# Kernel tuning notes

Hardware: AMD Instinct MI355X
Metric: run time of the kernel (lower is better)

Reference implementation:

```python
import jax, jax.numpy as jnp
import numpy as np

N = 50000        # nodes
E = 800000       # original edges (no self loops)
HEADS = 2
OUT = 64         # hidden_channels
NUM_GRAPHS = 128
NEG_SLOPE = 0.2


def setup_inputs() -> dict:
    key = jax.random.key(0)
    ks = jax.random.split(key, 16)
    # edge_index guaranteed free of self loops (remove_self_loops then add_self_loops
    # in the original makes the final edge set = original edges + N self loops)
    src = jax.random.randint(ks[0], (E,), 0, N)
    off = jax.random.randint(ks[1], (E,), 1, N)
    dst = (src + off) % N
    edge_index = jnp.stack([src, dst]).astype(jnp.int64)
    batch = jnp.sort(jax.random.randint(ks[2], (N,), 0, NUM_GRAPHS)).astype(jnp.int64)
    def glorot(k, shape):
        fan = shape[-1] + (shape[0] if len(shape) > 1 else shape[-1])
        s = jnp.sqrt(6.0 / fan)
        return jax.random.uniform(k, shape, jnp.float32, -s, s)
    return {
        "x": jax.random.normal(ks[3], (N, 128), jnp.float32),
        "edge_index": edge_index,
        "batch": batch,
        "node_centrality": jax.random.uniform(ks[4], (N,), jnp.float32),
        "edge_centrality": jax.random.uniform(ks[5], (E,), jnp.float32),
        "W0": glorot(ks[6], (128, HEADS * OUT)),
        "as0": glorot(ks[7], (HEADS, OUT)),
        "ad0": glorot(ks[8], (HEADS, OUT)),
        "b0": jnp.ones((HEADS * OUT,), jnp.float32),
        "W1": glorot(ks[9], (HEADS * OUT, HEADS * OUT)),
        "as1": glorot(ks[10], (HEADS, OUT)),
        "ad1": glorot(ks[11], (HEADS, OUT)),
        "b1": jnp.ones((HEADS * OUT,), jnp.float32),
        "Wc": glorot(ks[12], (HEADS * OUT, 10)),
        "bc": jnp.zeros((10,), jnp.float32),
    }


def qgat_layer(x, src, dst, norm_quantum, W, a_src, a_dst, b):
    # x: [N, Cin]; src/dst: [E+N]; norm_quantum: [E+N]
    h = (x @ W).reshape(N, HEADS, OUT)                      # [N,H,D]
    alpha_s = jnp.einsum('nhd,hd->nh', h, a_src)            # [N,H]
    alpha_d = jnp.einsum('nhd,hd->nh', h, a_dst)
    alpha = jax.nn.leaky_relu(alpha_s[src] + alpha_d[dst], NEG_SLOPE)  # [E+N,H]
    # segment softmax over destination node (every node has a self loop)
    amax = jax.ops.segment_max(alpha, dst, num_segments=N)
    amax = jnp.where(jnp.isfinite(amax), amax, 0.0)
    ex = jnp.exp(alpha - amax[dst])
    denom = jax.ops.segment_sum(ex, dst, num_segments=N)
    attn = ex / (denom[dst] + 1e-16)                        # [E+N,H]
    # message: norm_quantum * alpha * x_j, scatter-add to dst
    msg = norm_quantum[:, None, None] * attn[:, :, None] * h[src]
    out = jax.ops.segment_sum(msg, dst, num_segments=N)     # [N,H,D]
    return jax.nn.relu(out.reshape(N, HEADS * OUT) + b)


def reference(x, edge_index, batch, node_centrality, edge_centrality,
              W0, as0, ad0, b0, W1, as1, ad1, b1, Wc, bc):
    loop = jnp.arange(N, dtype=edge_index.dtype)
    src = jnp.concatenate([edge_index[0], loop])            # self loops appended
    dst = jnp.concatenate([edge_index[1], loop])
    nq = jnp.concatenate([edge_centrality, node_centrality])  # [E+N]
    # eval mode: dropout is identity
    h = qgat_layer(x, src, dst, nq, W0, as0, ad0, b0)
    h = qgat_layer(h, src, dst, nq, W1, as1, ad1, b1)
    # global mean pool over graphs in the batch
    sums = jax.ops.segment_sum(h, batch, num_segments=NUM_GRAPHS)
    cnts = jax.ops.segment_sum(jnp.ones((N,), h.dtype), batch, num_segments=NUM_GRAPHS)
    pooled = sums / jnp.maximum(cnts, 1.0)[:, None]         # [G, H*D]
    return pooled @ Wc + bc                                  # [G, 10]
```

## Files before the change

### kernel.cpp

```cpp
#include <hip/hip_runtime.h>

#define N_NODES 50000
#define E_EDGES 800000
#define EA (E_EDGES + N_NODES)
#define NG 128
#define NEG 0.2f
#define NB_SCAN ((N_NODES + 255) / 256)
#define PCH 64

typedef _Float16 half8  __attribute__((ext_vector_type(8)));
typedef _Float16 half2t __attribute__((ext_vector_type(2)));
typedef float    floatx4 __attribute__((ext_vector_type(4)));

__device__ __forceinline__ half2t h2bits(unsigned u) { return __builtin_bit_cast(half2t, u); }

__global__ void init_kernel(const float* __restrict__ W0, const float* __restrict__ W1,
                            _Float16* __restrict__ Wt0, _Float16* __restrict__ Wt1,
                            int* __restrict__ deg, float* __restrict__ sums) {
    int i = blockIdx.x * 256 + threadIdx.x;
    if (i < N_NODES) deg[i] = 0;
    if (i < NG * 128) sums[i] = 0.f;
    if (i < 16384) {
        int c = i >> 7, k = i & 127;
        Wt0[c * 128 + k] = (_Float16)W0[k * 128 + c];
        Wt1[c * 128 + k] = (_Float16)W1[k * 128 + c];
    }
}

__global__ void hist_kernel(const int* __restrict__ ei, int* __restrict__ deg,
                            int* __restrict__ rank) {
    int e = blockIdx.x * blockDim.x + threadIdx.x;
    if (e >= EA) return;
    int d = (e < E_EDGES) ? ei[E_EDGES + e] : (e - E_EDGES);
    rank[e] = atomicAdd(&deg[d], 1);
}

__global__ void partial_kernel(const int* __restrict__ deg, int* __restrict__ part) {
    __shared__ int buf[4];
    int i = blockIdx.x * 256 + threadIdx.x;
    int v = (i < N_NODES) ? deg[i] : 0;
    for (int o = 32; o; o >>= 1) v += __shfl_xor(v, o);
    if ((threadIdx.x & 63) == 0) buf[threadIdx.x >> 6] = v;
    __syncthreads();
    if (threadIdx.x == 0) part[blockIdx.x] = buf[0] + buf[1] + buf[2] + buf[3];
}

__global__ void rowstart_kernel(const int* __restrict__ deg, const int* __restrict__ part,
                                int* __restrict__ rowstart) {
    __shared__ int buf[256];
    __shared__ int wsum[4];
    __shared__ int offs;
    int t = threadIdx.x;
    int pv = (t < blockIdx.x) ? part[t] : 0;
    for (int o = 32; o; o >>= 1) pv += __shfl_xor(pv, o);
    if ((t & 63) == 0) wsum[t >> 6] = pv;
    __syncthreads();
    if (t == 0) offs = wsum[0] + wsum[1] + wsum[2] + wsum[3];
    int i = blockIdx.x * 256 + t;
    int v = (i < N_NODES) ? deg[i] : 0;
    buf[t] = v;
    __syncthreads();
    for (int o = 1; o < 256; o <<= 1) {
        int u = (t >= o) ? buf[t - o] : 0;
        __syncthreads();
        buf[t] += u;
        __syncthreads();
    }
    if (i < N_NODES) rowstart[i] = offs + buf[t] - v;
    if (i == N_NODES - 1) rowstart[N_NODES] = offs + buf[t];
}

__global__ void build_kernel(const int* __restrict__ ei, const float* __restrict__ ec,
                             const float* __restrict__ nc, const int* __restrict__ rowstart,
                             const int* __restrict__ rank, uint2* __restrict__ csr2) {
    int e = blockIdx.x * blockDim.x + threadIdx.x;
    if (e >= EA) return;
    int s, d; float nq;
    if (e < E_EDGES) { s = ei[e]; d = ei[E_EDGES + e]; nq = ec[e]; }
    else             { s = e - E_EDGES; d = s; nq = nc[s]; }
    csr2[rowstart[d] + rank[e]] = make_uint2((unsigned)s, __float_as_uint(nq));
}

template<int SRC_F32>
__global__ __launch_bounds__(256) void gemm_mfma(const void* __restrict__ Xsrc,
                                                 const _Float16* __restrict__ Wt,
                                                 const float* __restrict__ as_,
                                                 const float* __restrict__ ad_,
                                                 unsigned* __restrict__ Hb,
                                                 float* __restrict__ als,
                                                 float* __restrict__ ald) {
    __shared__ _Float16 As[64][136];
    __shared__ _Float16 Bs[128 * 128];
    __shared__ float als_s[4][64];
    __shared__ float ald_s[4][64];
    const int tid = threadIdx.x;
    const int row0 = blockIdx.x * 64;

    if (SRC_F32) {
        const float* X = (const float*)Xsrc;
        for (int i = 0; i < 8; ++i) {
            int idx = tid + i * 256;
            int r = idx >> 5, q = idx & 31;
            int gr = row0 + r;
            float4 v = make_float4(0.f, 0.f, 0.f, 0.f);
            if (gr < N_NODES) v = ((const float4*)X)[(size_t)gr * 32 + q];
            half2t p0 = { (_Float16)v.x, (_Float16)v.y };
            half2t p1 = { (_Float16)v.z, (_Float16)v.w };
            *(half2t*)&As[r][q * 4]     = p0;
            *(half2t*)&As[r][q * 4 + 2] = p1;
        }
    } else {
        const uint4* X = (const uint4*)Xsrc;
        for (int i = 0; i < 4; ++i) {
            int idx = tid + i * 256;
            int r = idx >> 4, q = idx & 15;
            int gr = row0 + r;
            uint4 v = make_uint4(0u, 0u, 0u, 0u);
            if (gr < N_NODES) v = X[(size_t)gr * 16 + q];
            *(uint4*)&As[r][q * 8] = v;
        }
    }
    for (int i = 0; i < 8; ++i) {
        int idx = tid + i * 256;
        int r = idx >> 4, q = idx & 15;
        *(uint4*)&Bs[r * 128 + ((q ^ (r & 15)) << 3)] = ((const uint4*)Wt)[r * 16 + q];
    }
    __syncthreads();

    const int l = tid & 63, wv = tid >> 6;
    const int c0w = wv * 32;
    const int lr = l & 15, lq = l >> 4;

    floatx4 acc[4][2];
#pragma unroll
    for (int m = 0; m < 4; ++m)
#pragma unroll
        for (int n = 0; n < 2; ++n) acc[m][n] = (floatx4){0.f, 0.f, 0.f, 0.f};

#pragma unroll
    for (int kk = 0; kk < 4; ++kk) {
        int kb = kk * 32 + lq * 8;
        int kg = (kk * 4 + lq) ^ lr;
        half8 a0 = *(const half8*)&As[lr][kb];
        half8 a1 = *(const half8*)&As[16 + lr][kb];
        half8 a2 = *(const half8*)&As[32 + lr][kb];
        half8 a3 = *(const half8*)&As[48 + lr][kb];
        half8 b0 = *(const half8*)&Bs[(c0w + lr) * 128 + (kg << 3)];
        half8 b1 = *(const half8*)&Bs[(c0w + 16 + lr) * 128 + (kg << 3)];
        acc[0][0] = __builtin_amdgcn_mfma_f32_16x16x32_f16(a0, b0, acc[0][0], 0, 0, 0);
        acc[1][0] = __builtin_amdgcn_mfma_f32_16x16x32_f16(a1, b0, acc[1][0], 0, 0, 0);
        acc[2][0] = __builtin_amdgcn_mfma_f32_16x16x32_f16(a2, b0, acc[2][0], 0, 0, 0);
        acc[3][0] = __builtin_amdgcn_mfma_f32_16x16x32_f16(a3, b0, acc[3][0], 0, 0, 0);
        acc[0][1] = __builtin_amdgcn_mfma_f32_16x16x32_f16(a0, b1, acc[0][1], 0, 0, 0);
        acc[1][1] = __builtin_amdgcn_mfma_f32_16x16x32_f16(a1, b1, acc[1][1], 0, 0, 0);
        acc[2][1] = __builtin_amdgcn_mfma_f32_16x16x32_f16(a2, b1, acc[2][1], 0, 0, 0);
        acc[3][1] = __builtin_amdgcn_mfma_f32_16x16x32_f16(a3, b1, acc[3][1], 0, 0, 0);
    }

    __syncthreads();

    float asv0 = as_[c0w + lr],      adv0 = ad_[c0w + lr];
    float asv1 = as_[c0w + 16 + lr], adv1 = ad_[c0w + 16 + lr];
#pragma unroll
    for (int m = 0; m < 4; ++m) {
#pragma unroll
        for (int reg = 0; reg < 4; ++reg) {
            float v0 = acc[m][0][reg];
            float v1 = acc[m][1][reg];
            int rl = 16 * m + 4 * lq + reg;
            _Float16* rowp = &As[rl][0];
            rowp[c0w + lr]      = (_Float16)v0;
            rowp[c0w + 16 + lr] = (_Float16)v1;
            float ss = v0 * asv0 + v1 * asv1;
            float dd = v0 * adv0 + v1 * adv1;
            ss += __shfl_xor(ss, 1); dd += __shfl_xor(dd, 1);
            ss += __shfl_xor(ss, 2); dd += __shfl_xor(dd, 2);
            ss += __shfl_xor(ss, 4); dd += __shfl_xor(dd, 4);
            ss += __shfl_xor(ss, 8); dd += __shfl_xor(dd, 8);
            if (lr == 0) { als_s[wv][rl] = ss; ald_s[wv][rl] = dd; }
        }
    }
    __syncthreads();

    for (int i = 0; i < 4; ++i) {
        int idx = tid + i * 256;
        int r = idx >> 4, q = idx & 15;
        int grow = row0 + r;
        if (grow < N_NODES) {
            uint4 v = *(uint4*)((unsigned short*)&As[r][0] + q * 8);
            ((uint4*)Hb)[(size_t)grow * 16 + q] = v;
        }
    }
    int r = tid & 63, sel = tid >> 6;
    int grow = row0 + r;
    if (grow < N_NODES) {
        if (sel == 0)      als[grow * 2 + 0] = als_s[0][r] + als_s[1][r];
        else if (sel == 1) als[grow * 2 + 1] = als_s[2][r] + als_s[3][r];
        else if (sel == 2) ald[grow * 2 + 0] = ald_s[0][r] + ald_s[1][r];
        else               ald[grow * 2 + 1] = ald_s[2][r] + ald_s[3][r];
    }
}

__global__ __launch_bounds__(256) void agg_kernel(const uint4* __restrict__ Hb4,
                                                  const uint2* __restrict__ csr2,
                                                  const float* __restrict__ als,
                                                  const float* __restrict__ ald,
                                                  const int* __restrict__ rowstart,
                                                  const float* __restrict__ bias,
                                                  _Float16* __restrict__ outp) {
    __shared__ uint4 sw[4][64];
    const int wv = threadIdx.x >> 6;
    int n = blockIdx.x * 4 + wv;
    if (n >= N_NODES) return;
    const int lane = threadIdx.x & 63;
    int start = rowstart[n], end = rowstart[n + 1];
    int deg = end - start;
    const float2* als2 = (const float2*)als;
    float2 adn = ((const float2*)ald)[n];

    int   s_reg  = n;
    float nq_reg = 0.f, a0_reg = -1e30f, a1_reg = -1e30f;
    if (lane < deg) {
        uint2 v = csr2[start + lane];
        s_reg  = (int)v.x;
        nq_reg = __uint_as_float(v.y);
        float2 av = als2[s_reg];
        float a0 = av.x + adn.x; a0_reg = (a0 > 0.f) ? a0 : NEG * a0;
        float a1 = av.y + adn.y; a1_reg = (a1 > 0.f) ? a1 : NEG * a1;
    }
    float m0 = a0_reg, m1 = a1_reg;
    for (int i = start + 64 + lane; i < end; i += 64) {
        uint2 v = csr2[i];
        float2 av = als2[v.x];
        float a0 = av.x + adn.x; a0 = (a0 > 0.f) ? a0 : NEG * a0;
        float a1 = av.y + adn.y; a1 = (a1 > 0.f) ? a1 : NEG * a1;
        m0 = fmaxf(m0, a0); m1 = fmaxf(m1, a1);
    }
    for (int o = 32; o; o >>= 1) { m0 = fmaxf(m0, __shfl_xor(m0, o)); m1 = fmaxf(m1, __shfl_xor(m1, o)); }

    float e0 = __expf(a0_reg - m0), e1 = __expf(a1_reg - m1);
    float s0 = e0, s1 = e1;
    for (int i = start + 64 + lane; i < end; i += 64) {
        uint2 v = csr2[i];
        float2 av = als2[v.x];
        float a0 = av.x + adn.x; a0 = (a0 > 0.f) ? a0 : NEG * a0;
        float a1 = av.y + adn.y; a1 = (a1 > 0.f) ? a1 : NEG * a1;
        s0 += __expf(a0 - m0); s1 += __expf(a1 - m1);
    }
    for (int o = 32; o; o >>= 1) { s0 += __shfl_xor(s0, o); s1 += __shfl_xor(s1, o); }
    float inv0 = 1.f / (s0 + 1e-16f), inv1 = 1.f / (s1 + 1e-16f);

    sw[wv][lane] = make_uint4((unsigned)s_reg,
                              __float_as_uint(nq_reg * e0 * inv0),
                              __float_as_uint(nq_reg * e1 * inv1), 0u);

    const int  c16   = lane & 15;
    const int  g     = lane >> 4;
    const bool head0 = (c16 < 8);
    float acc0 = 0.f, acc1 = 0.f, acc2 = 0.f, acc3 = 0.f;
    float acc4 = 0.f, acc5 = 0.f, acc6 = 0.f, acc7 = 0.f;
    int cnt4 = (deg < 64) ? ((deg + 3) & ~3) : 64;
#pragma unroll 4
    for (int jp = 0; jp < cnt4; jp += 4) {
        uint4 sv = sw[wv][jp + g];
        float w  = __uint_as_float(head0 ? sv.y : sv.z);
        uint4 hv = Hb4[(size_t)(sv.x * 16u + (unsigned)c16)];
        half2t h0 = h2bits(hv.x), h1 = h2bits(hv.y), h2 = h2bits(hv.z), h3 = h2bits(hv.w);
        acc0 += (float)h0.x * w; acc1 += (float)h0.y * w;
        acc2 += (float)h1.x * w; acc3 += (float)h1.y * w;
        acc4 += (float)h2.x * w; acc5 += (float)h2.y * w;
        acc6 += (float)h3.x * w; acc7 += (float)h3.y * w;
    }
    for (int cbase = start + 64; cbase < end; cbase += 64) {
        int   s2 = n; float w0f = 0.f, w1f = 0.f;
        int i = cbase + lane;
        if (i < end) {
            uint2 v = csr2[i];
            s2 = (int)v.x;
            float nq = __uint_as_float(v.y);
            float2 av = als2[s2];
            float a0 = av.x + adn.x; a0 = (a0 > 0.f) ? a0 : NEG * a0;
            float a1 = av.y + adn.y; a1 = (a1 > 0.f) ? a1 : NEG * a1;
            w0f = nq * __expf(a0 - m0) * inv0;
            w1f = nq * __expf(a1 - m1) * inv1;
        }
        sw[wv][lane] = make_uint4((unsigned)s2, __float_as_uint(w0f), __float_as_uint(w1f), 0u);
        int rem = end - cbase; if (rem > 64) rem = 64;
        int r4 = (rem + 3) & ~3;
        for (int jp = 0; jp < r4; jp += 4) {
            uint4 sv = sw[wv][jp + g];
            float w  = __uint_as_float(head0 ? sv.y : sv.z);
            uint4 hv = Hb4[(size_t)(sv.x * 16u + (unsigned)c16)];
            half2t h0 = h2bits(hv.x), h1 = h2bits(hv.y), h2 = h2bits(hv.z), h3 = h2bits(hv.w);
            acc0 += (float)h0.x * w; acc1 += (float)h0.y * w;
            acc2 += (float)h1.x * w; acc3 += (float)h1.y * w;
            acc4 += (float)h2.x * w; acc5 += (float)h2.y * w;
            acc6 += (float)h3.x * w; acc7 += (float)h3.y * w;
        }
    }
    acc0 += __shfl_xor(acc0, 16); acc1 += __shfl_xor(acc1, 16);
    acc2 += __shfl_xor(acc2, 16); acc3 += __shfl_xor(acc3, 16);
    acc4 += __shfl_xor(acc4, 16); acc5 += __shfl_xor(acc5, 16);
    acc6 += __shfl_xor(acc6, 16); acc7 += __shfl_xor(acc7, 16);
    acc0 += __shfl_xor(acc0, 32); acc1 += __shfl_xor(acc1, 32);
    acc2 += __shfl_xor(acc2, 32); acc3 += __shfl_xor(acc3, 32);
    acc4 += __shfl_xor(acc4, 32); acc5 += __shfl_xor(acc5, 32);
    acc6 += __shfl_xor(acc6, 32); acc7 += __shfl_xor(acc7, 32);

    if (g == 0) {
        float4 ba = ((const float4*)bias)[c16 * 2];
        float4 bb = ((const float4*)bias)[c16 * 2 + 1];
        float o0 = acc0 + ba.x; o0 = o0 > 0.f ? o0 : 0.f;
        float o1 = acc1 + ba.y; o1 = o1 > 0.f ? o1 : 0.f;
        float o2 = acc2 + ba.z; o2 = o2 > 0.f ? o2 : 0.f;
        float o3 = acc3 + ba.w; o3 = o3 > 0.f ? o3 : 0.f;
        float o4 = acc4 + bb.x; o4 = o4 > 0.f ? o4 : 0.f;
        float o5 = acc5 + bb.y; o5 = o5 > 0.f ? o5 : 0.f;
        float o6 = acc6 + bb.z; o6 = o6 > 0.f ? o6 : 0.f;
        float o7 = acc7 + bb.w; o7 = o7 > 0.f ? o7 : 0.f;
        half8 hv = { (_Float16)o0, (_Float16)o1, (_Float16)o2, (_Float16)o3,
                     (_Float16)o4, (_Float16)o5, (_Float16)o6, (_Float16)o7 };
        *(half8*)(outp + (size_t)n * 128 + 8 * c16) = hv;
    }
}

__global__ __launch_bounds__(256) void pool_partial(const half2t* __restrict__ Obh,
                                                    const int* __restrict__ batch,
                                                    float* __restrict__ sums) {
    int row0 = blockIdx.x * PCH;
    int c2 = threadIdx.x & 63;
    int r4 = threadIdx.x >> 6;
    int end = row0 + PCH; if (end > N_NODES) end = N_NODES;
    float a0 = 0.f, a1 = 0.f;
    int curg = -1;
    for (int i = row0 + r4; i < end; i += 4) {
        int g = batch[i];
        if (g != curg) {
            if (curg >= 0) {
                atomicAdd(&sums[curg * 128 + 2 * c2],     a0);
                atomicAdd(&sums[curg * 128 + 2 * c2 + 1], a1);
            }
            a0 = 0.f; a1 = 0.f; curg = g;
        }
        half2t hv = Obh[(size_t)i * 64 + c2];
        a0 += (float)hv.x;
        a1 += (float)hv.y;
    }
    if (curg >= 0) {
        atomicAdd(&sums[curg * 128 + 2 * c2],     a0);
        atomicAdd(&sums[curg * 128 + 2 * c2 + 1], a1);
    }
}

__global__ void cls_kernel(const float* __restrict__ sums, const int* __restrict__ batch,
                           const float* __restrict__ Wc, const float* __restrict__ bc,
                           float* __restrict__ outp) {
    int g = blockIdx.x;
    __shared__ float p[128];
    __shared__ int cnt_s;
    if (threadIdx.x == 0) {
        int lo = 0, hi = N_NODES;
        while (lo < hi) { int mid = (lo + hi) >> 1; if (batch[mid] < g) lo = mid + 1; else hi = mid; }
        int start = lo;
        hi = N_NODES;
        while (lo < hi) { int mid = (lo + hi) >> 1; if (batch[mid] <= g) lo = mid + 1; else hi = mid; }
        cnt_s = lo - start;
    }
    __syncthreads();
    float inv = 1.f / fmaxf((float)cnt_s, 1.f);
    p[threadIdx.x] = sums[g * 128 + threadIdx.x] * inv;
    __syncthreads();
    if (threadIdx.x < 10) {
        float acc = bc[threadIdx.x];
        for (int k = 0; k < 128; ++k) acc += p[k] * Wc[k * 10 + threadIdx.x];
        outp[g * 10 + threadIdx.x] = acc;
    }
}

extern "C" void kernel_launch(void* const* d_in, const int* in_sizes, int n_in,
                              void* d_out, int out_size, void* d_ws, size_t ws_size,
                              hipStream_t stream) {
    const float* x     = (const float*)d_in[0];
    const int*   ei    = (const int*)d_in[1];
    const int*   batch = (const int*)d_in[2];
    const float* nc    = (const float*)d_in[3];
    const float* ec    = (const float*)d_in[4];
    const float* W0    = (const float*)d_in[5];
    const float* as0   = (const float*)d_in[6];
    const float* ad0   = (const float*)d_in[7];
    const float* b0    = (const float*)d_in[8];
    const float* W1    = (const float*)d_in[9];
    const float* as1   = (const float*)d_in[10];
    const float* ad1   = (const float*)d_in[11];
    const float* b1    = (const float*)d_in[12];
    const float* Wc    = (const float*)d_in[13];
    const float* bc    = (const float*)d_in[14];
    float* out = (float*)d_out;

    char* ws = (char*)d_ws;
    size_t off = 0;
    auto alloc = [&](size_t bytes) { void* p = ws + off; off += (bytes + 255) & ~size_t(255); return p; };
    unsigned*  Hb       = (unsigned*)alloc(sizeof(unsigned) * N_NODES * 64);
    _Float16*  Xh       = (_Float16*)alloc(sizeof(_Float16) * N_NODES * 128);
    _Float16*  Ob       = (_Float16*)alloc(sizeof(_Float16) * N_NODES * 128);
    float*     als      = (float*)alloc(sizeof(float) * N_NODES * 2);
    float*     ald      = (float*)alloc(sizeof(float) * N_NODES * 2);
    _Float16*  Wt0      = (_Float16*)alloc(sizeof(_Float16) * 128 * 128);
    _Float16*  Wt1      = (_Float16*)alloc(sizeof(_Float16) * 128 * 128);
    int*       deg      = (int*)alloc(sizeof(int) * N_NODES);
    int*       rank     = (int*)alloc(sizeof(int) * EA);
    int*       part     = (int*)alloc(sizeof(int) * NB_SCAN);
    int*       rowstart = (int*)alloc(sizeof(int) * (N_NODES + 1));
    uint2*     csr2     = (uint2*)alloc(sizeof(uint2) * EA);
    float*     sums     = (float*)alloc(sizeof(float) * NG * 128);

    init_kernel<<<NB_SCAN, 256, 0, stream>>>(W0, W1, Wt0, Wt1, deg, sums);
    hist_kernel<<<(EA + 255) / 256, 256, 0, stream>>>(ei, deg, rank);
    partial_kernel<<<NB_SCAN, 256, 0, stream>>>(deg, part);
    rowstart_kernel<<<NB_SCAN, 256, 0, stream>>>(deg, part, rowstart);
    build_kernel<<<(EA + 255) / 256, 256, 0, stream>>>(ei, ec, nc, rowstart, rank, csr2);

    int gemm_grid   = (N_NODES + 63) / 64;
    int nwaveblocks = (N_NODES + 3) / 4;

    gemm_mfma<1><<<gemm_grid, 256, 0, stream>>>(x, Wt0, as0, ad0, Hb, als, ald);
    agg_kernel<<<nwaveblocks, 256, 0, stream>>>((const uint4*)Hb, csr2, als, ald, rowstart, b0, Xh);

    gemm_mfma<0><<<gemm_grid, 256, 0, stream>>>(Xh, Wt1, as1, ad1, Hb, als, ald);
    agg_kernel<<<nwaveblocks, 256, 0, stream>>>((const uint4*)Hb, csr2, als, ald, rowstart, b1, Ob);

    pool_partial<<<(N_NODES + PCH - 1) / PCH, 256, 0, stream>>>((const half2t*)Ob, batch, sums);
    cls_kernel<<<NG, 128, 0, stream>>>(sums, batch, Wc, bc, out);
}
```

Baseline: 197.9 us.

## Process two nodes per wavefront in GAT aggregation using half-waves

The aggregation kernel now assigns one node to each 32-lane half of a wavefront instead of a whole 64-lane wave, halving the grid size. With about 17 edges per node on average, most lanes of a full wave sat idle in the softmax and gather phases. The shuffle reductions shrink to 32 lanes and the gather loop processes two edges per step per half-wave. This trades fewer idle lanes for longer serial loops on high-degree nodes and divergence between the two halves. The bounds check is removed, which relies on N being divisible by 8.

```diff
diff --git a/kernel.cpp b/kernel.cpp
--- a/kernel.cpp
+++ b/kernel.cpp
@@ -209,10 +209,12 @@
                                                   const float* __restrict__ bias,
                                                   _Float16* __restrict__ outp) {
     __shared__ uint4 sw[4][64];
-    const int wv = threadIdx.x >> 6;
-    int n = blockIdx.x * 4 + wv;
-    if (n >= N_NODES) return;
+    const int wv   = threadIdx.x >> 6;
     const int lane = threadIdx.x & 63;
+    const int hl   = lane >> 5;
+    const int l32  = lane & 31;
+    const int n = blockIdx.x * 8 + wv * 2 + hl;
+
     int start = rowstart[n], end = rowstart[n + 1];
     int deg = end - start;
     const float2* als2 = (const float2*)als;
@@ -220,8 +222,8 @@
 
     int   s_reg  = n;
     float nq_reg = 0.f, a0_reg = -1e30f, a1_reg = -1e30f;
-    if (lane < deg) {
-        uint2 v = csr2[start + lane];
+    if (l32 < deg) {
+        uint2 v = csr2[start + l32];
         s_reg  = (int)v.x;
         nq_reg = __uint_as_float(v.y);
         float2 av = als2[s_reg];
@@ -229,40 +231,40 @@
         float a1 = av.y + adn.y; a1_reg = (a1 > 0.f) ? a1 : NEG * a1;
     }
     float m0 = a0_reg, m1 = a1_reg;
-    for (int i = start + 64 + lane; i < end; i += 64) {
+    for (int i = start + 32 + l32; i < end; i += 32) {
         uint2 v = csr2[i];
         float2 av = als2[v.x];
         float a0 = av.x + adn.x; a0 = (a0 > 0.f) ? a0 : NEG * a0;
         float a1 = av.y + adn.y; a1 = (a1 > 0.f) ? a1 : NEG * a1;
         m0 = fmaxf(m0, a0); m1 = fmaxf(m1, a1);
     }
-    for (int o = 32; o; o >>= 1) { m0 = fmaxf(m0, __shfl_xor(m0, o)); m1 = fmaxf(m1, __shfl_xor(m1, o)); }
+    for (int o = 16; o; o >>= 1) { m0 = fmaxf(m0, __shfl_xor(m0, o)); m1 = fmaxf(m1, __shfl_xor(m1, o)); }
 
     float e0 = __expf(a0_reg - m0), e1 = __expf(a1_reg - m1);
     float s0 = e0, s1 = e1;
-    for (int i = start + 64 + lane; i < end; i += 64) {
+    for (int i = start + 32 + l32; i < end; i += 32) {
         uint2 v = csr2[i];
         float2 av = als2[v.x];
         float a0 = av.x + adn.x; a0 = (a0 > 0.f) ? a0 : NEG * a0;
         float a1 = av.y + adn.y; a1 = (a1 > 0.f) ? a1 : NEG * a1;
         s0 += __expf(a0 - m0); s1 += __expf(a1 - m1);
     }
-    for (int o = 32; o; o >>= 1) { s0 += __shfl_xor(s0, o); s1 += __shfl_xor(s1, o); }
+    for (int o = 16; o; o >>= 1) { s0 += __shfl_xor(s0, o); s1 += __shfl_xor(s1, o); }
     float inv0 = 1.f / (s0 + 1e-16f), inv1 = 1.f / (s1 + 1e-16f);
 
-    sw[wv][lane] = make_uint4((unsigned)s_reg,
-                              __float_as_uint(nq_reg * e0 * inv0),
-                              __float_as_uint(nq_reg * e1 * inv1), 0u);
-
-    const int  c16   = lane & 15;
-    const int  g     = lane >> 4;
+    sw[wv][hl * 32 + l32] = make_uint4((unsigned)s_reg,
+                                       __float_as_uint(nq_reg * e0 * inv0),
+                                       __float_as_uint(nq_reg * e1 * inv1), 0u);
+
+    const int  c16   = l32 & 15;
+    const int  g     = l32 >> 4;
     const bool head0 = (c16 < 8);
     float acc0 = 0.f, acc1 = 0.f, acc2 = 0.f, acc3 = 0.f;
     float acc4 = 0.f, acc5 = 0.f, acc6 = 0.f, acc7 = 0.f;
-    int cnt4 = (deg < 64) ? ((deg + 3) & ~3) : 64;
-#pragma unroll 4
-    for (int jp = 0; jp < cnt4; jp += 4) {
-        uint4 sv = sw[wv][jp + g];
+    int cnt2 = (deg < 32) ? ((deg + 1) & ~1) : 32;
+#pragma unroll 8
+    for (int jp = 0; jp < cnt2; jp += 2) {
+        uint4 sv = sw[wv][hl * 32 + jp + g];
         float w  = __uint_as_float(head0 ? sv.y : sv.z);
         uint4 hv = Hb4[(size_t)(sv.x * 16u + (unsigned)c16)];
         half2t h0 = h2bits(hv.x), h1 = h2bits(hv.y), h2 = h2bits(hv.z), h3 = h2bits(hv.w);
@@ -271,9 +273,9 @@
         acc4 += (float)h2.x * w; acc5 += (float)h2.y * w;
         acc6 += (float)h3.x * w; acc7 += (float)h3.y * w;
     }
-    for (int cbase = start + 64; cbase < end; cbase += 64) {
+    for (int cbase = start + 32; cbase < end; cbase += 32) {
         int   s2 = n; float w0f = 0.f, w1f = 0.f;
-        int i = cbase + lane;
+        int i = cbase + l32;
         if (i < end) {
             uint2 v = csr2[i];
             s2 = (int)v.x;
@@ -284,11 +286,12 @@
             w0f = nq * __expf(a0 - m0) * inv0;
             w1f = nq * __expf(a1 - m1) * inv1;
         }
-        sw[wv][lane] = make_uint4((unsigned)s2, __float_as_uint(w0f), __float_as_uint(w1f), 0u);
-        int rem = end - cbase; if (rem > 64) rem = 64;
-        int r4 = (rem + 3) & ~3;
-        for (int jp = 0; jp < r4; jp += 4) {
-            uint4 sv = sw[wv][jp + g];
+        sw[wv][hl * 32 + l32] = make_uint4((unsigned)s2, __float_as_uint(w0f),
+                                           __float_as_uint(w1f), 0u);
+        int rem = end - cbase; if (rem > 32) rem = 32;
+        int r2 = (rem + 1) & ~1;
+        for (int jp = 0; jp < r2; jp += 2) {
+            uint4 sv = sw[wv][hl * 32 + jp + g];
             float w  = __uint_as_float(head0 ? sv.y : sv.z);
             uint4 hv = Hb4[(size_t)(sv.x * 16u + (unsigned)c16)];
             half2t h0 = h2bits(hv.x), h1 = h2bits(hv.y), h2 = h2bits(hv.z), h3 = h2bits(hv.w);
@@ -302,10 +305,6 @@
     acc2 += __shfl_xor(acc2, 16); acc3 += __shfl_xor(acc3, 16);
     acc4 += __shfl_xor(acc4, 16); acc5 += __shfl_xor(acc5, 16);
     acc6 += __shfl_xor(acc6, 16); acc7 += __shfl_xor(acc7, 16);
-    acc0 += __shfl_xor(acc0, 32); acc1 += __shfl_xor(acc1, 32);
-    acc2 += __shfl_xor(acc2, 32); acc3 += __shfl_xor(acc3, 32);
-    acc4 += __shfl_xor(acc4, 32); acc5 += __shfl_xor(acc5, 32);
-    acc6 += __shfl_xor(acc6, 32); acc7 += __shfl_xor(acc7, 32);
 
     if (g == 0) {
         float4 ba = ((const float4*)bias)[c16 * 2];
@@ -420,14 +419,14 @@
     rowstart_kernel<<<NB_SCAN, 256, 0, stream>>>(deg, part, rowstart);
     build_kernel<<<(EA + 255) / 256, 256, 0, stream>>>(ei, ec, nc, rowstart, rank, csr2);
 
-    int gemm_grid   = (N_NODES + 63) / 64;
-    int nwaveblocks = (N_NODES + 3) / 4;
+    int gemm_grid  = (N_NODES + 63) / 64;
+    int agg_blocks = N_NODES / 8;
 
     gemm_mfma<1><<<gemm_grid, 256, 0, stream>>>(x, Wt0, as0, ad0, Hb, als, ald);
-    agg_kernel<<<nwaveblocks, 256, 0, stream>>>((const uint4*)Hb, csr2, als, ald, rowstart, b0, Xh);
+    agg_kernel<<<agg_blocks, 256, 0, stream>>>((const uint4*)Hb, csr2, als, ald, rowstart, b0, Xh);
 
     gemm_mfma<0><<<gemm_grid, 256, 0, stream>>>(Xh, Wt1, as1, ad1, Hb, als, ald);
-    agg_kernel<<<nwaveblocks, 256, 0, stream>>>((const uint4*)Hb, csr2, als, ald, rowstart, b1, Ob);
+    agg_kernel<<<agg_blocks, 256, 0, stream>>>((const uint4*)Hb, csr2, als, ald, rowstart, b1, Ob);
 
     pool_partial<<<(N_NODES + PCH - 1) / PCH, 256, 0, stream>>>((const half2t*)Ob, batch, sums);
     cls_kernel<<<NG, 128, 0, stream>>>(sums, batch, Wc, bc, out);
```

Result: no change. 199.7 us (+0.9%).
